# Performance work log

Measured on AMD Instinct MI355X. Metric: run time of the kernel, lower is better.

The kernel has to match this reference:

```python
import jax, jax.numpy as jnp
import numpy as np

HEADS = 8
DIM_HEAD = 64
SCALE = DIM_HEAD ** -0.5


def setup_inputs() -> dict:
    key = jax.random.key(0)
    ks = jax.random.split(key, 6)
    b, n, dim, inner = 8, 1024, 512, HEADS * DIM_HEAD
    return {
        "x": jax.random.normal(ks[0], (b, n, dim), jnp.float32),
        "y": jax.random.normal(ks[1], (b, n, dim), jnp.float32),
        "wq": jax.random.normal(ks[2], (dim, inner), jnp.float32) * 0.02,
        "wkv": jax.random.normal(ks[3], (dim, 2 * inner), jnp.float32) * 0.02,
        "wout": jax.random.normal(ks[4], (inner, dim), jnp.float32) * 0.02,
        "bout": jnp.zeros((dim,), jnp.float32),
    }


def _split_heads(t):
    # [b, n, h*d] -> [b, h, n, d]
    b, n, hd = t.shape
    return t.reshape(b, n, HEADS, DIM_HEAD).transpose(0, 2, 1, 3)


def _merge_heads(t):
    # [b, h, n, d] -> [b, n, h*d]
    b, h, n, d = t.shape
    return t.transpose(0, 2, 1, 3).reshape(b, n, h * d)


def _cross_attn(q_in, kv_in, wq, wkv, wout, bout):
    # queries from q_in, keys/values from kv_in; top-(nk//4) masked softmax attention
    nk = kv_in.shape[1]
    q = _split_heads(q_in @ wq)                     # [b,h,nq,d]
    kv = kv_in @ wkv                                # [b,nk,2*inner]
    k, v = jnp.split(kv, 2, axis=-1)
    k, v = _split_heads(k), _split_heads(v)         # [b,h,nk,d]
    dots = jnp.einsum('bhid,bhjd->bhij', q, k) * SCALE  # [b,h,nq,nk]
    kk = max(nk // 4, 1)
    kth = jax.lax.top_k(dots, kk)[0][..., -1:]      # k-th largest per row
    masked = jnp.where(dots >= kth, dots, -jnp.inf)
    attn = jax.nn.softmax(masked, axis=-1)
    out = jnp.einsum('bhij,bhjd->bhid', attn, v)
    return _merge_heads(out) @ wout + bout


def reference(x, y, wq, wkv, wout, bout):
    out_y = _cross_attn(y, x, wq, wkv, wout, bout)  # y attends to x
    out_x = _cross_attn(x, y, wq, wkv, wout, bout)  # x attends to y
    return (out_x, out_y)
```

## Files before the change

### kernel.cpp

```cpp
#include <hip/hip_runtime.h>
#include <hip/hip_bf16.h>

typedef __attribute__((ext_vector_type(8))) short bfx8;
typedef __attribute__((ext_vector_type(4))) float fx4;

__device__ __forceinline__ short f2bf(float f) {
    union { float f; unsigned u; } v; v.f = f;
    unsigned r = v.u + 0x7fffu + ((v.u >> 16) & 1u);
    return (short)(r >> 16);
}
__device__ __forceinline__ float bf2f(short b) {
    union { unsigned u; float f; } v; v.u = ((unsigned)(unsigned short)b) << 16; return v.f;
}

__global__ __launch_bounds__(256) void proj_kernel(
    const float* __restrict__ X, const float* __restrict__ Y,
    const float* __restrict__ wq, const float* __restrict__ wkv,
    short* __restrict__ QpX, short* __restrict__ KpX, short* __restrict__ VbX,
    short* __restrict__ QpY, short* __restrict__ KpY, short* __restrict__ VbY)
{
    const int inp = blockIdx.z;
    const float* A = inp ? Y : X;
    short* Qp = inp ? QpY : QpX;
    short* Kp = inp ? KpY : KpX;
    short* Vb = inp ? VbY : VbX;
    const int mb = blockIdx.x;
    const int nb = blockIdx.y;
    const int tid = threadIdx.x;
    const int lane = tid & 63;
    const int w = tid >> 6, wm = w >> 1, wn = w & 1;
    const int l15 = lane & 15, g8 = (lane >> 4) * 8;

    __shared__ short As[128][72];
    __shared__ short Bs[128][72];

    const float* Bsrc; int ldb, nbase0;
    if (nb < 4) { Bsrc = wq;  ldb = 512;  nbase0 = nb * 128; }
    else        { Bsrc = wkv; ldb = 1024; nbase0 = nb * 128 - 512; }

    fx4 acc[4][4];
    const fx4 z4 = {0.f, 0.f, 0.f, 0.f};
    for (int i = 0; i < 4; i++) for (int j = 0; j < 4; j++) acc[i][j] = z4;

    const int arow = tid >> 1, ahalf = (tid & 1) * 16;
    const int bk = tid >> 3, bnseg = (tid & 7) * 16;

    for (int kb = 0; kb < 512; kb += 32) {
        __syncthreads();
        {
            const float* src = A + (size_t)(mb * 128 + arow) * 512 + kb + ahalf;
            bfx8 h0, h1, l0, l1;
            #pragma unroll
            for (int q = 0; q < 4; q++) {
                float4 v = *(const float4*)(src + q * 4);
                float vv[4] = {v.x, v.y, v.z, v.w};
                #pragma unroll
                for (int c = 0; c < 4; c++) {
                    int idx = q * 4 + c;
                    short h = f2bf(vv[c]);
                    short l = f2bf(vv[c] - bf2f(h));
                    if (idx < 8) { h0[idx] = h; l0[idx] = l; }
                    else         { h1[idx - 8] = h; l1[idx - 8] = l; }
                }
            }
            *(bfx8*)&As[arow][ahalf] = h0;      *(bfx8*)&As[arow][ahalf + 8] = h1;
            *(bfx8*)&As[arow][32 + ahalf] = l0; *(bfx8*)&As[arow][32 + ahalf + 8] = l1;
        }
        {
            const float* src = Bsrc + (size_t)(kb + bk) * ldb + nbase0 + bnseg;
            #pragma unroll
            for (int q = 0; q < 4; q++) {
                float4 v = *(const float4*)(src + q * 4);
                float vv[4] = {v.x, v.y, v.z, v.w};
                #pragma unroll
                for (int c = 0; c < 4; c++) {
                    int n = bnseg + q * 4 + c;
                    short h = f2bf(vv[c]);
                    Bs[n][bk] = h;
                    Bs[n][32 + bk] = f2bf(vv[c] - bf2f(h));
                }
            }
        }
        __syncthreads();
        bfx8 ah[4], al[4], bh[4], bl[4];
        #pragma unroll
        for (int mt = 0; mt < 4; mt++) {
            int r = wm * 64 + mt * 16 + l15;
            ah[mt] = *(bfx8*)&As[r][g8];
            al[mt] = *(bfx8*)&As[r][32 + g8];
        }
        #pragma unroll
        for (int nt = 0; nt < 4; nt++) {
            int r = wn * 64 + nt * 16 + l15;
            bh[nt] = *(bfx8*)&Bs[r][g8];
            bl[nt] = *(bfx8*)&Bs[r][32 + g8];
        }
        #pragma unroll
        for (int mt = 0; mt < 4; mt++)
            #pragma unroll
            for (int nt = 0; nt < 4; nt++) {
                acc[mt][nt] = __builtin_amdgcn_mfma_f32_16x16x32_bf16(ah[mt], bh[nt], acc[mt][nt], 0, 0, 0);
                acc[mt][nt] = __builtin_amdgcn_mfma_f32_16x16x32_bf16(ah[mt], bl[nt], acc[mt][nt], 0, 0, 0);
                acc[mt][nt] = __builtin_amdgcn_mfma_f32_16x16x32_bf16(al[mt], bh[nt], acc[mt][nt], 0, 0, 0);
            }
    }
    #pragma unroll
    for (int mt = 0; mt < 4; mt++)
        #pragma unroll
        for (int nt = 0; nt < 4; nt++)
            #pragma unroll
            for (int r = 0; r < 4; r++) {
                int row = mb * 128 + wm * 64 + mt * 16 + (lane >> 4) * 4 + r;
                int col = nb * 128 + wn * 64 + nt * 16 + l15;
                float v = acc[mt][nt][r];
                int b = row >> 10, n = row & 1023;
                if (col < 512) {
                    v *= 0.125f;
                    int h = col >> 6, d = col & 63;
                    size_t base = ((size_t)(b * 8 + h) * 1024 + n) * 128;
                    short hi = f2bf(v);
                    Qp[base + d] = hi;
                    Qp[base + 64 + d] = f2bf(v - bf2f(hi));
                } else if (col < 1024) {
                    int cc = col - 512;
                    int h = cc >> 6, d = cc & 63;
                    size_t base = ((size_t)(b * 8 + h) * 1024 + n) * 128;
                    short hi = f2bf(v);
                    Kp[base + d] = hi;
                    Kp[base + 64 + d] = f2bf(v - bf2f(hi));
                } else {
                    Vb[(size_t)row * 512 + (col - 1024)] = f2bf(v);
                }
            }
}

__global__ __launch_bounds__(256) void transv_kernel(
    const short* __restrict__ VbX, const short* __restrict__ VbY,
    short* __restrict__ VtX, short* __restrict__ VtY)
{
    const int inp = blockIdx.z;
    const short* Vb = inp ? VbY : VbX;
    short* Vt = inp ? VtY : VtX;
    const int bh = blockIdx.y, b = bh >> 3, h = bh & 7;
    const int nt = blockIdx.x;
    const int tid = threadIdx.x;
    __shared__ short tile[64][66];
    {
        int r = tid >> 2, c0 = (tid & 3) * 16;
        const short* src = Vb + ((size_t)(b * 1024 + nt * 64 + r)) * 512 + h * 64 + c0;
        bfx8 v0 = *(const bfx8*)src;
        bfx8 v1 = *(const bfx8*)(src + 8);
        #pragma unroll
        for (int i = 0; i < 8; i++) { tile[r][c0 + i] = v0[i]; tile[r][c0 + 8 + i] = v1[i]; }
    }
    __syncthreads();
    {
        int d = tid >> 2, n0 = (tid & 3) * 16;
        bfx8 o0, o1;
        #pragma unroll
        for (int i = 0; i < 8; i++) { o0[i] = tile[n0 + i][d]; o1[i] = tile[n0 + 8 + i][d]; }
        short* dst = Vt + ((size_t)(bh * 64 + d)) * 1024 + nt * 64 + n0;
        *(bfx8*)dst = o0;
        *(bfx8*)(dst + 8) = o1;
    }
}

#define PBUF_BYTES 32768
#define HIST_OFF   32768
#define PMX_OFF    38912
#define PMN_OFF    39424
#define PSUM_OFF   39936
#define RMX_OFF    40448
#define RMN_OFF    40512
#define RT_OFF     40576
#define RB_OFF     40640
#define RN_OFF     40704
#define RC_OFF     40768
#define ATTN_LDS   40832

__global__ __launch_bounds__(512, 4) void attn_kernel(
    const short* __restrict__ QpX, const short* __restrict__ KpX, const short* __restrict__ VtX,
    const short* __restrict__ QpY, const short* __restrict__ KpY, const short* __restrict__ VtY,
    short* __restrict__ inner)
{
    extern __shared__ char smem[];
    unsigned* histU  = (unsigned*)(smem + HIST_OFF);
    float*    candF  = (float*)(smem + HIST_OFF);
    float*    psumPV = (float*)(smem + HIST_OFF);
    float*    partmx = (float*)(smem + PMX_OFF);
    float*    partmn = (float*)(smem + PMN_OFF);
    float*    partsum= (float*)(smem + PSUM_OFF);
    float*    rowMx  = (float*)(smem + RMX_OFF);
    float*    rowMn  = (float*)(smem + RMN_OFF);
    float*    rowT   = (float*)(smem + RT_OFF);
    int*      rowB   = (int*)(smem + RB_OFF);
    int*      rowNeed= (int*)(smem + RN_OFF);
    int*      rowcnt = (int*)(smem + RC_OFF);

    const int dir = blockIdx.z;
    const short* Qp = dir ? QpY : QpX;
    const short* Kp = dir ? KpX : KpY;
    const short* Vt = dir ? VtX : VtY;
    const int bh = blockIdx.y;
    const int qb = blockIdx.x;
    const int tid = threadIdx.x;
    const int lane = tid & 63;
    const int w = tid >> 6;
    const int l15 = lane & 15, g = lane >> 4;

    bfx8 qf[2][2];
    {
        const short* qbase = Qp + ((size_t)bh * 1024 + qb * 16 + l15) * 128;
        #pragma unroll
        for (int ks = 0; ks < 2; ks++)
            #pragma unroll
            for (int p = 0; p < 2; p++)
                qf[ks][p] = *(const bfx8*)(qbase + p * 64 + ks * 32 + g * 8);
    }

    fx4 acc[8];
    {
        const fx4 z4 = {0.f, 0.f, 0.f, 0.f};
        #pragma unroll
        for (int t = 0; t < 8; t++) acc[t] = z4;
        const short* kbase = Kp + ((size_t)bh * 1024 + w * 128 + l15) * 128 + g * 8;
        bfx8 kh0 = *(const bfx8*)(kbase);
        bfx8 kh1 = *(const bfx8*)(kbase + 32);
        bfx8 kl0 = *(const bfx8*)(kbase + 64);
        bfx8 kl1 = *(const bfx8*)(kbase + 96);
        #pragma unroll
        for (int t = 0; t < 8; t++) {
            bfx8 nh0, nh1, nl0, nl1;
            if (t < 7) {
                const short* nb = kbase + (t + 1) * 2048;
                nh0 = *(const bfx8*)(nb);
                nh1 = *(const bfx8*)(nb + 32);
                nl0 = *(const bfx8*)(nb + 64);
                nl1 = *(const bfx8*)(nb + 96);
            }
            acc[t] = __builtin_amdgcn_mfma_f32_16x16x32_bf16(qf[0][0], kh0, acc[t], 0, 0, 0);
            acc[t] = __builtin_amdgcn_mfma_f32_16x16x32_bf16(qf[0][0], kl0, acc[t], 0, 0, 0);
            acc[t] = __builtin_amdgcn_mfma_f32_16x16x32_bf16(qf[0][1], kh0, acc[t], 0, 0, 0);
            acc[t] = __builtin_amdgcn_mfma_f32_16x16x32_bf16(qf[1][0], kh1, acc[t], 0, 0, 0);
            acc[t] = __builtin_amdgcn_mfma_f32_16x16x32_bf16(qf[1][0], kl1, acc[t], 0, 0, 0);
            acc[t] = __builtin_amdgcn_mfma_f32_16x16x32_bf16(qf[1][1], kh1, acc[t], 0, 0, 0);
            kh0 = nh0; kh1 = nh1; kl0 = nl0; kl1 = nl1;
        }
    }

    #pragma unroll
    for (int r = 0; r < 4; r++) {
        float a = acc[0][r], b = acc[0][r];
        #pragma unroll
        for (int t = 1; t < 8; t++) { a = fmaxf(a, acc[t][r]); b = fminf(b, acc[t][r]); }
        #pragma unroll
        for (int o = 1; o < 16; o <<= 1) { a = fmaxf(a, __shfl_xor(a, o)); b = fminf(b, __shfl_xor(b, o)); }
        if (l15 == 0) {
            int lrow = g * 4 + r;
            partmx[lrow * 8 + w] = a;
            partmn[lrow * 8 + w] = b;
        }
    }
    for (int i = tid; i < 16 * 96; i += 512) histU[i] = 0;
    if (tid < 16) rowcnt[tid] = 0;
    __syncthreads();

    float mxr[4], mnr[4], invr[4];
    #pragma unroll
    for (int r = 0; r < 4; r++) {
        int lrow = g * 4 + r;
        float a = partmx[lrow * 8 + 0], b = partmn[lrow * 8 + 0];
        #pragma unroll
        for (int j = 1; j < 8; j++) { a = fmaxf(a, partmx[lrow * 8 + j]); b = fminf(b, partmn[lrow * 8 + j]); }
        mxr[r] = a; mnr[r] = b;
        invr[r] = (a - b > 1e-30f) ? 96.0f / (a - b) : 0.0f;
        if (w == 0 && l15 == 0) { rowMx[lrow] = a; rowMn[lrow] = b; }
    }
    #pragma unroll
    for (int r = 0; r < 4; r++) {
        int lrow = g * 4 + r;
        #pragma unroll
        for (int t = 0; t < 8; t++) {
            int bin = (int)((acc[t][r] - mnr[r]) * invr[r]);
            bin = bin < 0 ? 0 : (bin > 95 ? 95 : bin);
            atomicAdd(&histU[lrow * 96 + bin], 1u);
        }
    }
    __syncthreads();

    #pragma unroll
    for (int rr = 0; rr < 2; rr++) {
        int row = w * 2 + rr;
        unsigned c0 = 0, c1 = 0;
        if (lane < 48) { c0 = histU[row * 96 + 2 * lane]; c1 = histU[row * 96 + 2 * lane + 1]; }
        unsigned ts = c0 + c1;
        #pragma unroll
        for (int o = 1; o < 64; o <<= 1) {
            unsigned u = __shfl_down(ts, o);
            if (lane + o < 64) ts += u;
        }
        unsigned ca_lo = ts - c0, ca_hi = ts - c0 - c1;
        bool oklo = (lane < 48) && (ca_lo < 256u) && (ca_lo + c0 >= 256u);
        bool okhi = (lane < 48) && (ca_hi < 256u) && (ca_hi + c1 >= 256u);
        unsigned long long bal = __ballot(oklo || okhi);
        int sl = __ffsll((long long)bal) - 1;
        int myB = oklo ? 2 * lane : 2 * lane + 1;
        int myNeed = 256 - (int)(oklo ? ca_lo : ca_hi);
        int B = __shfl(myB, sl);
        int need = __shfl(myNeed, sl);
        if (lane == 0) {
            float mr = rowMx[row], nr = rowMn[row];
            if (mr - nr < 1e-30f) { rowB[row] = -1; rowT[row] = nr; rowNeed[row] = 1; }
            else { rowB[row] = B; rowNeed[row] = need; }
        }
    }
    __syncthreads();

    #pragma unroll
    for (int r = 0; r < 4; r++) {
        int lrow = g * 4 + r;
        int B = rowB[lrow];
        #pragma unroll
        for (int t = 0; t < 8; t++) {
            int bin = (int)((acc[t][r] - mnr[r]) * invr[r]);
            bin = bin < 0 ? 0 : (bin > 95 ? 95 : bin);
            if (B >= 0 && bin == B) {
                int idx = atomicAdd(&rowcnt[lrow], 1);
                if (idx < 64) candF[lrow * 64 + idx] = acc[t][r];
            }
        }
    }
    __syncthreads();

    #pragma unroll
    for (int rr = 0; rr < 2; rr++) {
        int row = w * 2 + rr;
        int B = rowB[row];
        if (B < 0) continue;
        int m = rowcnt[row]; m = m > 64 ? 64 : m;
        int need = rowNeed[row];
        const float* crow = candF + row * 64;
        float v0 = (lane < m) ? crow[lane] : 0.f;
        int cg = 0, ce = 0;
        for (int i = 0; i < m; i++) {
            float c = crow[i];
            cg += (c > v0); ce += (c == v0);
        }
        bool ok = (lane < m) && (cg < need) && (need <= cg + ce);
        unsigned long long bal = __ballot(ok);
        float tt;
        if (bal) tt = __shfl(v0, __ffsll((long long)bal) - 1);
        else     tt = rowMn[row] + (float)B * (rowMx[row] - rowMn[row]) * (1.0f / 96.0f);
        if (lane == 0) rowT[row] = tt;
    }
    __syncthreads();

    #pragma unroll
    for (int r = 0; r < 4; r++) {
        int lrow = g * 4 + r;
        float tthr = rowT[lrow];
        float s = 0.f;
        unsigned sw = (unsigned)((lrow & 7) << 4);
        #pragma unroll
        for (int t = 0; t < 8; t++) {
            float v = acc[t][r];
            float p = (v >= tthr) ? __expf(v - mxr[r]) : 0.f;
            s += p;
            int col = w * 128 + t * 16 + l15;
            *(short*)(smem + (size_t)lrow * 2048 + (((unsigned)(col * 2)) ^ sw)) = f2bf(p);
        }
        #pragma unroll
        for (int o = 1; o < 16; o <<= 1) s += __shfl_xor(s, o);
        if (l15 == 0) partsum[lrow * 8 + w] = s;
    }
    __syncthreads();

    {
        const int ws = w & 3;
        const int kh = w >> 2;
        const short* vrow = Vt + ((size_t)bh * 64 + ws * 16 + l15) * 1024 + kh * 512;
        const char* pbase = smem + (size_t)l15 * 2048;
        const unsigned sw = (unsigned)((l15 & 7) << 4);
        fx4 acc0 = {0.f, 0.f, 0.f, 0.f}, acc1 = {0.f, 0.f, 0.f, 0.f};
        #pragma unroll
        for (int ks = 0; ks < 16; ks += 2) {
            bfx8 pa0 = *(const bfx8*)(pbase + (((unsigned)(kh * 1024 + ks * 64 + g * 16)) ^ sw));
            bfx8 vv0 = *(const bfx8*)(vrow + ks * 32 + g * 8);
            bfx8 pa1 = *(const bfx8*)(pbase + (((unsigned)(kh * 1024 + (ks + 1) * 64 + g * 16)) ^ sw));
            bfx8 vv1 = *(const bfx8*)(vrow + (ks + 1) * 32 + g * 8);
            acc0 = __builtin_amdgcn_mfma_f32_16x16x32_bf16(pa0, vv0, acc0, 0, 0, 0);
            acc1 = __builtin_amdgcn_mfma_f32_16x16x32_bf16(pa1, vv1, acc1, 0, 0, 0);
        }
        if (kh == 1) {
            float4 pv;
            pv.x = acc0[0] + acc1[0]; pv.y = acc0[1] + acc1[1];
            pv.z = acc0[2] + acc1[2]; pv.w = acc0[3] + acc1[3];
            *(float4*)&psumPV[(ws * 64 + lane) * 4] = pv;
        }
        __syncthreads();
        if (kh == 0) {
            const float4 other = *(const float4*)&psumPV[(ws * 64 + lane) * 4];
            float oth[4] = {other.x, other.y, other.z, other.w};
            #pragma unroll
            for (int r = 0; r < 4; r++) {
                int qrow = g * 4 + r;
                float denom = partsum[qrow * 8 + 0] + partsum[qrow * 8 + 1] +
                              partsum[qrow * 8 + 2] + partsum[qrow * 8 + 3] +
                              partsum[qrow * 8 + 4] + partsum[qrow * 8 + 5] +
                              partsum[qrow * 8 + 6] + partsum[qrow * 8 + 7];
                float v = (acc0[r] + acc1[r] + oth[r]) / denom;
                size_t orow = (size_t)dir * 8192 + (size_t)(bh >> 3) * 1024 + qb * 16 + qrow;
                inner[orow * 512 + (bh & 7) * 64 + ws * 16 + l15] = f2bf(v);
            }
        }
    }
}

__global__ __launch_bounds__(256) void outproj_kernel(
    const short* __restrict__ inner, const float* __restrict__ wout,
    const float* __restrict__ bout, float* __restrict__ out)
{
    const int mb = blockIdx.x;
    const int nb = blockIdx.y;
    const int tid = threadIdx.x;
    const int lane = tid & 63;
    const int w = tid >> 6, wm = w >> 1, wn = w & 1;
    const int l15 = lane & 15, g8 = (lane >> 4) * 8;

    __shared__ short As[128][40];
    __shared__ short Bs[128][40];

    fx4 acc[4][4];
    const fx4 z4 = {0.f, 0.f, 0.f, 0.f};
    for (int i = 0; i < 4; i++) for (int j = 0; j < 4; j++) acc[i][j] = z4;

    const int arow = tid >> 1, ahalf = (tid & 1) * 16;
    const int bk = tid >> 3, bnseg = (tid & 7) * 16;

    for (int kb = 0; kb < 512; kb += 32) {
        __syncthreads();
        {
            const short* src = inner + (size_t)(mb * 128 + arow) * 512 + kb + ahalf;
            bfx8 v0 = *(const bfx8*)src, v1 = *(const bfx8*)(src + 8);
            *(bfx8*)&As[arow][ahalf] = v0;
            *(bfx8*)&As[arow][ahalf + 8] = v1;
        }
        {
            const float* src = wout + (size_t)(kb + bk) * 512 + nb * 128 + bnseg;
            #pragma unroll
            for (int q = 0; q < 4; q++) {
                float4 v = *(const float4*)(src + q * 4);
                float vv[4] = {v.x, v.y, v.z, v.w};
                #pragma unroll
                for (int c = 0; c < 4; c++) Bs[bnseg + q * 4 + c][bk] = f2bf(vv[c]);
            }
        }
        __syncthreads();
        bfx8 af[4], bf[4];
        #pragma unroll
        for (int mt = 0; mt < 4; mt++) af[mt] = *(bfx8*)&As[wm * 64 + mt * 16 + l15][g8];
        #pragma unroll
        for (int nt = 0; nt < 4; nt++) bf[nt] = *(bfx8*)&Bs[wn * 64 + nt * 16 + l15][g8];
        #pragma unroll
        for (int mt = 0; mt < 4; mt++)
            #pragma unroll
            for (int nt = 0; nt < 4; nt++)
                acc[mt][nt] = __builtin_amdgcn_mfma_f32_16x16x32_bf16(af[mt], bf[nt], acc[mt][nt], 0, 0, 0);
    }
    #pragma unroll
    for (int mt = 0; mt < 4; mt++)
        #pragma unroll
        for (int nt = 0; nt < 4; nt++)
            #pragma unroll
            for (int r = 0; r < 4; r++) {
                int row = mb * 128 + wm * 64 + mt * 16 + (lane >> 4) * 4 + r;
                int col = nb * 128 + wn * 64 + nt * 16 + l15;
                out[(size_t)row * 512 + col] = acc[mt][nt][r] + bout[col];
            }
}

extern "C" void kernel_launch(void* const* d_in, const int* in_sizes, int n_in,
                              void* d_out, int out_size, void* d_ws, size_t ws_size,
                              hipStream_t stream)
{
    const float* x    = (const float*)d_in[0];
    const float* y    = (const float*)d_in[1];
    const float* wq   = (const float*)d_in[2];
    const float* wkv  = (const float*)d_in[3];
    const float* wout = (const float*)d_in[4];
    const float* bout = (const float*)d_in[5];
    float* out = (float*)d_out;

    char* ws = (char*)d_ws;
    size_t off = 0;
    auto alloc = [&](size_t bytes) -> void* {
        void* p = ws + off; off += (bytes + 255) & ~(size_t)255; return p;
    };
    const size_t QP = (size_t)8 * 8 * 1024 * 128 * 2;
    const size_t VB = (size_t)8192 * 512 * 2;
    short* QpX = (short*)alloc(QP);
    short* KpX = (short*)alloc(QP);
    short* QpY = (short*)alloc(QP);
    short* KpY = (short*)alloc(QP);
    short* VbX = (short*)alloc(VB);
    short* VbY = (short*)alloc(VB);
    short* VtX = (short*)alloc(VB);
    short* VtY = (short*)alloc(VB);
    short* inner = (short*)alloc((size_t)2 * 8192 * 512 * 2);
    if (off > ws_size) return;

    proj_kernel<<<dim3(64, 12, 2), 256, 0, stream>>>(x, y, wq, wkv, QpX, KpX, VbX, QpY, KpY, VbY);
    transv_kernel<<<dim3(16, 64, 2), 256, 0, stream>>>(VbX, VbY, VtX, VtY);
    (void)hipFuncSetAttribute((const void*)attn_kernel,
                              hipFuncAttributeMaxDynamicSharedMemorySize, ATTN_LDS);
    attn_kernel<<<dim3(64, 64, 2), 512, ATTN_LDS, stream>>>(QpX, KpX, VtX, QpY, KpY, VtY, inner);
    outproj_kernel<<<dim3(128, 4, 1), 256, 0, stream>>>(inner, wout, bout, out);
}
```

Before: 799.3 us.

## Permute V layout to match packed P stores, use DPP row reductions, pad LDS

Stores each thread's eight softmax probabilities as one packed 16-byte LDS write instead of eight scalar short stores. To keep P·V correct, the K-dimension order of P changes, and the V transpose kernel writes Vt in a matching permuted column order. Cross-lane max, min and sum reductions across 16 lanes now use DPP row operations instead of shuffles. The histogram and candidate LDS arrays get padded strides to reduce bank conflicts. The risk is that the P columns and permuted V columns must line up exactly with the MFMA operand layout.

```diff
diff --git a/kernel.cpp b/kernel.cpp
--- a/kernel.cpp
+++ b/kernel.cpp
@@ -2,6 +2,7 @@
 #include <hip/hip_bf16.h>
 
 typedef __attribute__((ext_vector_type(8))) short bfx8;
+typedef __attribute__((ext_vector_type(4))) short sx4;
 typedef __attribute__((ext_vector_type(4))) float fx4;
 
 __device__ __forceinline__ short f2bf(float f) {
@@ -11,6 +12,26 @@
 }
 __device__ __forceinline__ float bf2f(short b) {
     union { unsigned u; float f; } v; v.u = ((unsigned)(unsigned short)b) << 16; return v.f;
+}
+
+template<int CTRL>
+__device__ __forceinline__ float dppf(float x) {
+    return __int_as_float(__builtin_amdgcn_update_dpp(0, __float_as_int(x), CTRL, 0xF, 0xF, false));
+}
+__device__ __forceinline__ float rowmax16(float a) {
+    a = fmaxf(a, dppf<0x121>(a)); a = fmaxf(a, dppf<0x122>(a));
+    a = fmaxf(a, dppf<0x124>(a)); a = fmaxf(a, dppf<0x128>(a));
+    return a;
+}
+__device__ __forceinline__ float rowmin16(float a) {
+    a = fminf(a, dppf<0x121>(a)); a = fminf(a, dppf<0x122>(a));
+    a = fminf(a, dppf<0x124>(a)); a = fminf(a, dppf<0x128>(a));
+    return a;
+}
+__device__ __forceinline__ float rowsum16(float a) {
+    a += dppf<0x121>(a); a += dppf<0x122>(a);
+    a += dppf<0x124>(a); a += dppf<0x128>(a);
+    return a;
 }
 
 __global__ __launch_bounds__(256) void proj_kernel(
@@ -155,28 +176,33 @@
     }
     __syncthreads();
     {
-        int d = tid >> 2, n0 = (tid & 3) * 16;
-        bfx8 o0, o1;
-        #pragma unroll
-        for (int i = 0; i < 8; i++) { o0[i] = tile[n0 + i][d]; o1[i] = tile[n0 + 8 + i][d]; }
-        short* dst = Vt + ((size_t)(bh * 64 + d)) * 1024 + nt * 64 + n0;
-        *(bfx8*)dst = o0;
-        *(bfx8*)(dst + 8) = o1;
-    }
-}
-
-#define PBUF_BYTES 32768
+        const int d = tid >> 2, jj = tid & 3;
+        const int w = nt >> 1, thalf = (nt & 1) * 4;
+        short* dstrow = Vt + ((size_t)(bh * 64 + d)) * 1024 + w * 128 + thalf;
+        #pragma unroll
+        for (int it = 0; it < 4; ++it) {
+            int l15 = (jj << 2) | it;
+            sx4 v;
+            v[0] = tile[l15][d];
+            v[1] = tile[16 + l15][d];
+            v[2] = tile[32 + l15][d];
+            v[3] = tile[48 + l15][d];
+            *(sx4*)(dstrow + l15 * 8) = v;
+        }
+    }
+}
+
 #define HIST_OFF   32768
-#define PMX_OFF    38912
-#define PMN_OFF    39424
-#define PSUM_OFF   39936
-#define RMX_OFF    40448
-#define RMN_OFF    40512
-#define RT_OFF     40576
-#define RB_OFF     40640
-#define RN_OFF     40704
-#define RC_OFF     40768
-#define ATTN_LDS   40832
+#define PMX_OFF    38976
+#define PMN_OFF    39488
+#define PSUM_OFF   40000
+#define RMX_OFF    40512
+#define RMN_OFF    40576
+#define RT_OFF     40640
+#define RB_OFF     40704
+#define RN_OFF     40768
+#define RC_OFF     40832
+#define ATTN_LDS   40896
 
 __global__ __launch_bounds__(512, 4) void attn_kernel(
     const short* __restrict__ QpX, const short* __restrict__ KpX, const short* __restrict__ VtX,
@@ -253,15 +279,14 @@
         float a = acc[0][r], b = acc[0][r];
         #pragma unroll
         for (int t = 1; t < 8; t++) { a = fmaxf(a, acc[t][r]); b = fminf(b, acc[t][r]); }
-        #pragma unroll
-        for (int o = 1; o < 16; o <<= 1) { a = fmaxf(a, __shfl_xor(a, o)); b = fminf(b, __shfl_xor(b, o)); }
+        a = rowmax16(a); b = rowmin16(b);
         if (l15 == 0) {
             int lrow = g * 4 + r;
             partmx[lrow * 8 + w] = a;
             partmn[lrow * 8 + w] = b;
         }
     }
-    for (int i = tid; i < 16 * 96; i += 512) histU[i] = 0;
+    for (int i = tid; i < 16 * 97; i += 512) histU[i] = 0;
     if (tid < 16) rowcnt[tid] = 0;
     __syncthreads();
 
@@ -283,7 +308,7 @@
         for (int t = 0; t < 8; t++) {
             int bin = (int)((acc[t][r] - mnr[r]) * invr[r]);
             bin = bin < 0 ? 0 : (bin > 95 ? 95 : bin);
-            atomicAdd(&histU[lrow * 96 + bin], 1u);
+            atomicAdd(&histU[lrow * 97 + bin], 1u);
         }
     }
     __syncthreads();
@@ -292,7 +317,7 @@
     for (int rr = 0; rr < 2; rr++) {
         int row = w * 2 + rr;
         unsigned c0 = 0, c1 = 0;
-        if (lane < 48) { c0 = histU[row * 96 + 2 * lane]; c1 = histU[row * 96 + 2 * lane + 1]; }
+        if (lane < 48) { c0 = histU[row * 97 + 2 * lane]; c1 = histU[row * 97 + 2 * lane + 1]; }
         unsigned ts = c0 + c1;
         #pragma unroll
         for (int o = 1; o < 64; o <<= 1) {
@@ -326,7 +351,7 @@
             bin = bin < 0 ? 0 : (bin > 95 ? 95 : bin);
             if (B >= 0 && bin == B) {
                 int idx = atomicAdd(&rowcnt[lrow], 1);
-                if (idx < 64) candF[lrow * 64 + idx] = acc[t][r];
+                if (idx < 64) candF[lrow * 65 + idx] = acc[t][r];
             }
         }
     }
@@ -339,7 +364,7 @@
         if (B < 0) continue;
         int m = rowcnt[row]; m = m > 64 ? 64 : m;
         int need = rowNeed[row];
-        const float* crow = candF + row * 64;
+        const float* crow = candF + row * 65;
         float v0 = (lane < m) ? crow[lane] : 0.f;
         int cg = 0, ce = 0;
         for (int i = 0; i < m; i++) {
@@ -360,17 +385,17 @@
         int lrow = g * 4 + r;
         float tthr = rowT[lrow];
         float s = 0.f;
-        unsigned sw = (unsigned)((lrow & 7) << 4);
+        bfx8 pk;
         #pragma unroll
         for (int t = 0; t < 8; t++) {
             float v = acc[t][r];
             float p = (v >= tthr) ? __expf(v - mxr[r]) : 0.f;
             s += p;
-            int col = w * 128 + t * 16 + l15;
-            *(short*)(smem + (size_t)lrow * 2048 + (((unsigned)(col * 2)) ^ sw)) = f2bf(p);
-        }
-        #pragma unroll
-        for (int o = 1; o < 16; o <<= 1) s += __shfl_xor(s, o);
+            pk[t] = f2bf(p);
+        }
+        unsigned sw = (unsigned)((lrow & 7) << 4);
+        *(bfx8*)(smem + (size_t)lrow * 2048 + (((unsigned)(w * 256 + l15 * 16)) ^ sw)) = pk;
+        s = rowsum16(s);
         if (l15 == 0) partsum[lrow * 8 + w] = s;
     }
     __syncthreads();
```

Result: no change. 789.6 us (-1.2%).
